# Performance work log

Measured on AMD Instinct MI355X. Metric: run time of the kernel, lower is better.

## Reference

```python
import jax, jax.numpy as jnp
import numpy as np

B, T, D = 64, 512, 1024

def setup_inputs() -> dict:
    key = jax.random.key(0)
    k1, k2, k3 = jax.random.split(key, 3)
    q1 = jax.random.normal(k1, (B, T, D), dtype=jnp.float32)
    q2 = jax.random.normal(k2, (B, T, D), dtype=jnp.float32)
    # original uses 'uniform' init; scale like a small uniform weight
    U = jax.random.uniform(k3, (D, D), dtype=jnp.float32, minval=-0.05, maxval=0.05)
    return {"q1": q1, "q2": q2, "U": U}

def reference(q1, q2, U):
    # bilinear scores: (q1 @ U) @ q2^T -> [B, T1, T2]
    att = jnp.einsum('btd,de,bse->bts', q1, U, q2)
    att = jax.nn.relu(att)
    w1_att = jax.nn.softmax(att, axis=1)  # softmax over q1 timesteps
    w2_att = jax.nn.softmax(att, axis=2)  # softmax over q2 timesteps
    # q1_align = w1_att^T @ q1 -> [B, T2, D]
    q1_align = jnp.einsum('bts,btd->bsd', w1_att, q1)
    # q2_align = w2_att @ q2 -> [B, T1, D]
    q2_align = jnp.einsum('bts,bsd->btd', w2_att, q2)
    return (q1_align, q2_align)
```

## Files before the change

kernel.cpp:

```cpp
#include <hip/hip_runtime.h>
#include <hip/hip_bf16.h>
#include <math.h>

#define B_DIM 64
#define T_DIM 512
#define D_DIM 1024
#define TT (T_DIM * T_DIM)
#define TD (T_DIM * D_DIM)

typedef _Float16 f16;
typedef f16 f16x4 __attribute__((ext_vector_type(4)));
typedef f16 f16x8 __attribute__((ext_vector_type(8)));
typedef float f32x4 __attribute__((ext_vector_type(4)));


__device__ __forceinline__ void gld_lds16(const void* g, void* l) {
    __builtin_amdgcn_global_load_lds(
        (const __attribute__((address_space(1))) void*)g,
        (__attribute__((address_space(3))) void*)l, 16, 0, 0);
}

template <int EPI>
__global__ __launch_bounds__(512, 2) void k_mfma2(
        const f16* __restrict__ A, int lda,
        const f16* __restrict__ Bt, int ldb, int K,
        void* __restrict__ Cout, int ldc,
        const float* __restrict__ scale,
        long batchA, long batchB, long batchC, long batchS,
        float2* __restrict__ rowP, float2* __restrict__ colP, long pstr,
        const f16* __restrict__ A2, const f16* __restrict__ Bt2,
        void* __restrict__ Cout2, const float* __restrict__ scale2, int zsplit) {
    __shared__ f16 LA[2][8192];
    __shared__ f16 LB[2][8192];

    const int tid = threadIdx.x;
    const int lane = tid & 63, w = tid >> 6;

    const int gX = gridDim.x, gY = gridDim.y;
    int nwg = gX * gY * gridDim.z;
    int o = blockIdx.x + gX * (blockIdx.y + gY * blockIdx.z);
    int q8 = nwg >> 3, r8 = nwg & 7, xcd = o & 7, idx = o >> 3;
    int fl = (xcd < r8 ? xcd * (q8 + 1) : r8 * (q8 + 1) + (xcd - r8) * q8) + idx;
    const int bx = fl % gX;
    int tmp = fl / gX;
    const int by = tmp % gY;
    const int bz = tmp / gY;

    const f16* Au = A; const f16* Bu = Bt;
    void* Cu = Cout; const float* su = scale;
    int zb = bz;
    if constexpr (EPI == 2) {
        if (bz >= zsplit) {
            zb = bz - zsplit;
            Au = A2; Bu = Bt2; Cu = Cout2; su = scale2;
        }
    }

    const f16* Ab = Au + (long)zb * batchA + (long)(by * 256) * lda;
    const f16* Bb = Bu + (long)zb * batchB + (long)(bx * 256) * ldb;

    const int r0 = tid >> 2, s0 = (tid & 3) ^ (r0 & 3);
    const int r1 = (512 + tid) >> 2, s1 = ((512 + tid) & 3) ^ (r1 & 3);
    const long offA0 = (long)r0 * lda + s0 * 8;
    const long offA1 = (long)r1 * lda + s1 * 8;
    const long offB0 = (long)r0 * ldb + s0 * 8;
    const long offB1 = (long)r1 * ldb + s1 * 8;
    const int ldsOff0 = w * 512;
    const int ldsOff1 = 4096 + w * 512;

    const int g = lane >> 4;
    const int rA0 = (w & 1) * 128 + (lane & 15);
    const int rB0 = (w >> 1) * 64 + (lane & 15);

    f32x4 acc[8][4] = {};

    gld_lds16(Ab + offA0, &LA[0][ldsOff0]);
    gld_lds16(Ab + offA1, &LA[0][ldsOff1]);
    gld_lds16(Bb + offB0, &LB[0][ldsOff0]);
    gld_lds16(Bb + offB1, &LB[0][ldsOff1]);
    __syncthreads();

    const int NT = K >> 5;
    for (int t = 0; t < NT; ++t) {
        const int cur = t & 1;
        if (t + 1 < NT) {
            const long kt = (long)(t + 1) << 5;
            gld_lds16(Ab + offA0 + kt, &LA[cur ^ 1][ldsOff0]);
            gld_lds16(Ab + offA1 + kt, &LA[cur ^ 1][ldsOff1]);
            gld_lds16(Bb + offB0 + kt, &LB[cur ^ 1][ldsOff0]);
            gld_lds16(Bb + offB1 + kt, &LB[cur ^ 1][ldsOff1]);
        }
        f16x8 a[8], b[4];
#pragma unroll
        for (int m = 0; m < 8; ++m) {
            int r = rA0 + m * 16;
            a[m] = *(const f16x8*)(&LA[cur][r * 32 + ((g ^ (r & 3)) << 3)]);
        }
#pragma unroll
        for (int n = 0; n < 4; ++n) {
            int r = rB0 + n * 16;
            b[n] = *(const f16x8*)(&LB[cur][r * 32 + ((g ^ (r & 3)) << 3)]);
        }
#pragma unroll
        for (int m = 0; m < 8; ++m)
#pragma unroll
            for (int n = 0; n < 4; ++n)
                acc[m][n] = __builtin_amdgcn_mfma_f32_16x16x32_f16(a[m], b[n], acc[m][n], 0, 0, 0);
        __syncthreads();
    }

    const int row0 = by * 256 + (w & 1) * 128 + (lane >> 4) * 4;
    const int col0 = bx * 256 + (w >> 1) * 64 + (lane & 15);

    if constexpr (EPI == 0) {
        f16* C = (f16*)Cu;
#pragma unroll
        for (int m = 0; m < 8; ++m)
#pragma unroll
            for (int r = 0; r < 4; ++r) {
                long row = row0 + m * 16 + r;
#pragma unroll
                for (int n = 0; n < 4; ++n)
                    C[row * ldc + col0 + n * 16] = (f16)acc[m][n][r];
            }
    } else if constexpr (EPI == 1) {
#pragma unroll
        for (int m = 0; m < 8; ++m)
#pragma unroll
            for (int n = 0; n < 4; ++n)
#pragma unroll
                for (int r = 0; r < 4; ++r)
                    acc[m][n][r] = fmaxf(acc[m][n][r], 0.0f);
        float* C = (float*)Cu + (long)zb * batchC;
#pragma unroll
        for (int m = 0; m < 8; ++m)
#pragma unroll
            for (int r = 0; r < 4; ++r) {
                long row = row0 + m * 16 + r;
#pragma unroll
                for (int n = 0; n < 4; ++n)
                    C[row * ldc + col0 + n * 16] = acc[m][n][r];
            }
        float* redR = (float*)(&LA[0][0]);
        float* redC = redR + 2048;
        const int h = w & 1, cw = w >> 1;
#pragma unroll
        for (int m = 0; m < 8; ++m)
#pragma unroll
            for (int r = 0; r < 4; ++r) {
                float mx = fmaxf(fmaxf(acc[m][0][r], acc[m][1][r]),
                                 fmaxf(acc[m][2][r], acc[m][3][r]));
                mx = fmaxf(mx, __shfl_xor(mx, 1));
                mx = fmaxf(mx, __shfl_xor(mx, 2));
                mx = fmaxf(mx, __shfl_xor(mx, 4));
                mx = fmaxf(mx, __shfl_xor(mx, 8));
                float sm = __expf(acc[m][0][r] - mx) + __expf(acc[m][1][r] - mx)
                         + __expf(acc[m][2][r] - mx) + __expf(acc[m][3][r] - mx);
                sm += __shfl_xor(sm, 1);
                sm += __shfl_xor(sm, 2);
                sm += __shfl_xor(sm, 4);
                sm += __shfl_xor(sm, 8);
                if ((lane & 15) == 0) {
                    int lr = m * 16 + (lane >> 4) * 4 + r;
                    redR[((h * 128 + lr) * 4 + cw) * 2 + 0] = mx;
                    redR[((h * 128 + lr) * 4 + cw) * 2 + 1] = sm;
                }
            }
#pragma unroll
        for (int n = 0; n < 4; ++n) {
            float mx = acc[0][n][0];
#pragma unroll
            for (int m = 0; m < 8; ++m)
#pragma unroll
                for (int r = 0; r < 4; ++r) mx = fmaxf(mx, acc[m][n][r]);
            mx = fmaxf(mx, __shfl_xor(mx, 16));
            mx = fmaxf(mx, __shfl_xor(mx, 32));
            float sm = 0.f;
#pragma unroll
            for (int m = 0; m < 8; ++m)
#pragma unroll
                for (int r = 0; r < 4; ++r) sm += __expf(acc[m][n][r] - mx);
            sm += __shfl_xor(sm, 16);
            sm += __shfl_xor(sm, 32);
            if (lane < 16) {
                int c = cw * 64 + n * 16 + lane;
                redC[(h * 256 + c) * 2 + 0] = mx;
                redC[(h * 256 + c) * 2 + 1] = sm;
            }
        }
        __syncthreads();
        if (tid < 256) {
            float M = -1e30f, S = 0.f;
#pragma unroll
            for (int i = 0; i < 4; ++i) {
                float m_ = redR[(tid * 4 + i) * 2 + 0];
                float s_ = redR[(tid * 4 + i) * 2 + 1];
                float nm = fmaxf(M, m_);
                S = S * __expf(M - nm) + s_ * __expf(m_ - nm);
                M = nm;
            }
            rowP[(long)bx * pstr + (long)bz * 512 + by * 256 + tid] = make_float2(M, S);
        } else {
            int c = tid - 256;
            float m0_ = redC[c * 2 + 0], s0_ = redC[c * 2 + 1];
            float m1_ = redC[(256 + c) * 2 + 0], s1_ = redC[(256 + c) * 2 + 1];
            float M = fmaxf(m0_, m1_);
            float S = s0_ * __expf(m0_ - M) + s1_ * __expf(m1_ - M);
            colP[(long)by * pstr + (long)bz * 512 + bx * 256 + c] = make_float2(M, S);
        }
    } else {
        float* C = (float*)Cu + (long)zb * batchC;
        const float* sz = su + (long)zb * batchS;
#pragma unroll
        for (int m = 0; m < 8; ++m)
#pragma unroll
            for (int r = 0; r < 4; ++r) {
                long row = row0 + m * 16 + r;
                float inv = 1.0f / sz[row];
#pragma unroll
                for (int n = 0; n < 4; ++n)
                    C[row * ldc + col0 + n * 16] = acc[m][n][r] * inv;
            }
    }
}

__global__ __launch_bounds__(256) void k_comb(const float2* __restrict__ rowP,
                                              const float2* __restrict__ colP, long pstr,
                                              float* __restrict__ rmax, float* __restrict__ rsum,
                                              float* __restrict__ cmax, float* __restrict__ csum,
                                              int b0, int n) {
    int i = blockIdx.x * 256 + threadIdx.x;
    if (i >= n) return;
    float2 a = rowP[i], b = rowP[pstr + i];
    float M = fmaxf(a.x, b.x);
    float S = a.y * __expf(a.x - M) + b.y * __expf(b.x - M);
    rmax[(size_t)b0 * T_DIM + i] = M;
    rsum[(size_t)b0 * T_DIM + i] = S;
    a = colP[i]; b = colP[pstr + i];
    M = fmaxf(a.x, b.x);
    S = a.y * __expf(a.x - M) + b.y * __expf(b.x - M);
    cmax[(size_t)b0 * T_DIM + i] = M;
    csum[(size_t)b0 * T_DIM + i] = S;
}

__global__ __launch_bounds__(256) void k_cast_both(const float* __restrict__ src,
                                                   f16* __restrict__ dst,
                                                   f16* __restrict__ dstT) {
    __shared__ f16 tr[64][72];
    int b = blockIdx.z;
    int d0 = blockIdx.x * 64, t0 = blockIdx.y * 64;
    const float* S = src + ((size_t)b * T_DIM + t0) * D_DIM + d0;
    f16* Dr = dst + ((size_t)b * T_DIM + t0) * D_DIM + d0;
    int tid = threadIdx.x;
    int rr = tid >> 4, cc = (tid & 15) * 4;
#pragma unroll
    for (int i = 0; i < 4; ++i) {
        int r = rr + i * 16;
        float4 v = *(const float4*)(S + (size_t)r * D_DIM + cc);
        f16x4 h = {(f16)v.x, (f16)v.y, (f16)v.z, (f16)v.w};
        *(f16x4*)(Dr + (size_t)r * D_DIM + cc) = h;
        tr[cc + 0][r] = h[0];
        tr[cc + 1][r] = h[1];
        tr[cc + 2][r] = h[2];
        tr[cc + 3][r] = h[3];
    }
    __syncthreads();
    f16* Dt = dstT + ((size_t)b * D_DIM + d0) * T_DIM + t0;
    int r2 = tid >> 3, c8 = (tid & 7) * 8;
#pragma unroll
    for (int i = 0; i < 2; ++i) {
        int d = r2 + i * 32;
        f16x8 vv = *(const f16x8*)(&tr[d][c8]);
        *(f16x8*)(Dt + (size_t)d * T_DIM + c8) = vv;
    }
}

__global__ __launch_bounds__(256) void k_castU(const float* __restrict__ U,
                                               f16* __restrict__ Uht) {
    __shared__ f16 tr[64][72];
    int n0 = blockIdx.x * 64, k0 = blockIdx.y * 64;
    int tid = threadIdx.x;
    int rr = tid >> 4, cc = (tid & 15) * 4;
#pragma unroll
    for (int i = 0; i < 4; ++i) {
        int r = rr + i * 16;
        float4 v = *(const float4*)(U + (size_t)(k0 + r) * D_DIM + n0 + cc);
        tr[cc + 0][r] = (f16)v.x;
        tr[cc + 1][r] = (f16)v.y;
        tr[cc + 2][r] = (f16)v.z;
        tr[cc + 3][r] = (f16)v.w;
    }
    __syncthreads();
    int r2 = tid >> 3, c8 = (tid & 7) * 8;
#pragma unroll
    for (int i = 0; i < 2; ++i) {
        int n = r2 + i * 32;
        f16x8 vv = *(const f16x8*)(&tr[n][c8]);
        *(f16x8*)(Uht + (size_t)(n0 + n) * D_DIM + k0 + c8) = vv;
    }
}

__global__ __launch_bounds__(256) void k_pconv(const float* __restrict__ att,
                                               const float* __restrict__ rmax,
                                               const float* __restrict__ cmax,
                                               f16* __restrict__ P2, f16* __restrict__ P1,
                                               int b0) {
    __shared__ f16 tr[64][72];
    int z = blockIdx.z;
    int t0 = blockIdx.y * 64, s0 = blockIdx.x * 64;
    const float* S = att + (size_t)z * TT + (size_t)t0 * T_DIM + s0;
    const float* rm = rmax + (size_t)(b0 + z) * T_DIM + t0;
    const float* cm = cmax + (size_t)(b0 + z) * T_DIM + s0;
    int tid = threadIdx.x;
    int rr = tid >> 4, cc = (tid & 15) * 4;
#pragma unroll
    for (int i = 0; i < 4; ++i) {
        int r = rr + i * 16;
        float4 v = *(const float4*)(S + (size_t)r * T_DIM + cc);
        float m = rm[r];
        f16x4 p2 = {(f16)__expf(v.x - m), (f16)__expf(v.y - m),
                    (f16)__expf(v.z - m), (f16)__expf(v.w - m)};
        *(f16x4*)(P2 + (size_t)z * TT + (size_t)(t0 + r) * T_DIM + s0 + cc) = p2;
        float4 c4 = *(const float4*)(cm + cc);
        tr[cc + 0][r] = (f16)__expf(v.x - c4.x);
        tr[cc + 1][r] = (f16)__expf(v.y - c4.y);
        tr[cc + 2][r] = (f16)__expf(v.z - c4.z);
        tr[cc + 3][r] = (f16)__expf(v.w - c4.w);
    }
    __syncthreads();
    int r2 = tid >> 3, c8 = (tid & 7) * 8;
#pragma unroll
    for (int i = 0; i < 2; ++i) {
        int s = r2 + i * 32;
        f16x8 vv = *(const f16x8*)(&tr[s][c8]);
        *(f16x8*)(P1 + (size_t)z * TT + (size_t)(s0 + s) * T_DIM + t0 + c8) = vv;
    }
}

__global__ __launch_bounds__(256) void k_rowstats(const float* __restrict__ att,
                                                  float* __restrict__ rmax,
                                                  float* __restrict__ rsum, int b0) {
    int wave = threadIdx.x >> 6, lane = threadIdx.x & 63;
    int lr = blockIdx.x * 4 + wave;
    const float4* row = reinterpret_cast<const float4*>(att + (size_t)lr * T_DIM);
    float4 v0 = row[lane];
    float4 v1 = row[lane + 64];
    float m = fmaxf(fmaxf(fmaxf(v0.x, v0.y), fmaxf(v0.z, v0.w)),
                    fmaxf(fmaxf(v1.x, v1.y), fmaxf(v1.z, v1.w)));
#pragma unroll
    for (int off = 32; off >= 1; off >>= 1) m = fmaxf(m, __shfl_xor(m, off));
    float s = __expf(v0.x - m) + __expf(v0.y - m) + __expf(v0.z - m) + __expf(v0.w - m)
            + __expf(v1.x - m) + __expf(v1.y - m) + __expf(v1.z - m) + __expf(v1.w - m);
#pragma unroll
    for (int off = 32; off >= 1; off >>= 1) s += __shfl_xor(s, off);
    if (lane == 0) {
        size_t gr = (size_t)b0 * T_DIM + lr;
        rmax[gr] = m;
        rsum[gr] = s;
    }
}

__global__ __launch_bounds__(256) void k_colstats(const float* __restrict__ att,
                                                  float* __restrict__ cmax,
                                                  float* __restrict__ csum, int b0) {
    int lb = blockIdx.y;
    int s = blockIdx.x * 256 + threadIdx.x;
    const float* base = att + (size_t)lb * TT + s;
    float m = -INFINITY, sum = 0.f;
    for (int t = 0; t < T_DIM; ++t) {
        float x = base[(size_t)t * T_DIM];
        float nm = fmaxf(m, x);
        sum = sum * __expf(m - nm) + __expf(x - nm);
        m = nm;
    }
    size_t g = (size_t)(b0 + lb) * T_DIM + s;
    cmax[g] = m;
    csum[g] = sum;
}

#define BM 128
#define BN 128
#define BKK 16
#define APITCH 132

__device__ __forceinline__ void stage_a_rowmajor(float* As, const float* __restrict__ A,
                                                 int lda, int tid) {
#pragma unroll
    for (int i = 0; i < 2; ++i) {
        int idx = tid + i * 256;
        int r = idx >> 2;
        int k4 = (idx & 3) << 2;
        float4 v = *reinterpret_cast<const float4*>(&A[(size_t)r * lda + k4]);
        As[(k4 + 0) * APITCH + r] = v.x;
        As[(k4 + 1) * APITCH + r] = v.y;
        As[(k4 + 2) * APITCH + r] = v.z;
        As[(k4 + 3) * APITCH + r] = v.w;
    }
}
__device__ __forceinline__ void stage_a_rowmajor_exp(float* As, const float* __restrict__ A,
                                                     int lda, const float* __restrict__ rowmax,
                                                     int tid) {
#pragma unroll
    for (int i = 0; i < 2; ++i) {
        int idx = tid + i * 256;
        int r = idx >> 2;
        int k4 = (idx & 3) << 2;
        float4 v = *reinterpret_cast<const float4*>(&A[(size_t)r * lda + k4]);
        float m = rowmax[r];
        As[(k4 + 0) * APITCH + r] = __expf(v.x - m);
        As[(k4 + 1) * APITCH + r] = __expf(v.y - m);
        As[(k4 + 2) * APITCH + r] = __expf(v.z - m);
        As[(k4 + 3) * APITCH + r] = __expf(v.w - m);
    }
}
__device__ __forceinline__ void stage_a_colmajor_exp(float* As, const float* __restrict__ S,
                                                     int lds, const float* __restrict__ colmax,
                                                     int tid) {
#pragma unroll
    for (int i = 0; i < 2; ++i) {
        int idx = tid + i * 256;
        int k = idx >> 5;
        int m4 = (idx & 31) << 2;
        float4 v = *reinterpret_cast<const float4*>(&S[(size_t)k * lds + m4]);
        float4 c = *reinterpret_cast<const float4*>(&colmax[m4]);
        float4 o;
        o.x = __expf(v.x - c.x); o.y = __expf(v.y - c.y);
        o.z = __expf(v.z - c.z); o.w = __expf(v.w - c.w);
        *reinterpret_cast<float4*>(&As[k * APITCH + m4]) = o;
    }
}
__device__ __forceinline__ void stage_b_rowmajor(float* Bs, const float* __restrict__ Bp,
                                                 int ldb, int tid) {
#pragma unroll
    for (int i = 0; i < 2; ++i) {
        int idx = tid + i * 256;
        int k = idx >> 5;
        int c4 = idx & 31;
        float4 v = *reinterpret_cast<const float4*>(&Bp[(size_t)k * ldb + (c4 << 2)]);
        *reinterpret_cast<float4*>(&Bs[k * BN + ((c4 & 1) << 6) + ((c4 >> 1) << 2)]) = v;
    }
}
__device__ __forceinline__ void stage_b_transpose(float* Bs, const float* __restrict__ Q,
                                                  int ldq, int tid) {
#pragma unroll
    for (int i = 0; i < 2; ++i) {
        int idx = tid + i * 256;
        int s = idx >> 2;
        int e4 = (idx & 3) << 2;
        float4 v = *reinterpret_cast<const float4*>(&Q[(size_t)s * ldq + e4]);
        int sw = ((s & 4) << 4) + ((s >> 3) << 2) + (s & 3);
        Bs[(e4 + 0) * BN + sw] = v.x;
        Bs[(e4 + 1) * BN + sw] = v.y;
        Bs[(e4 + 2) * BN + sw] = v.z;
        Bs[(e4 + 3) * BN + sw] = v.w;
    }
}
__device__ __forceinline__ void gemm_inner(const float* As, const float* Bs,
                                           float acc[8][8], int tx, int ty) {
#pragma unroll
    for (int k = 0; k < BKK; ++k) {
        float4 a0 = *reinterpret_cast<const float4*>(&As[k * APITCH + ty * 8]);
        float4 a1 = *reinterpret_cast<const float4*>(&As[k * APITCH + ty * 8 + 4]);
        float4 b0 = *reinterpret_cast<const float4*>(&Bs[k * BN + tx * 4]);
        float4 b1 = *reinterpret_cast<const float4*>(&Bs[k * BN + 64 + tx * 4]);
        float a[8] = {a0.x, a0.y, a0.z, a0.w, a1.x, a1.y, a1.z, a1.w};
        float b[8] = {b0.x, b0.y, b0.z, b0.w, b1.x, b1.y, b1.z, b1.w};
#pragma unroll
        for (int i = 0; i < 8; ++i)
#pragma unroll
            for (int j = 0; j < 8; ++j)
                acc[i][j] = fmaf(a[i], b[j], acc[i][j]);
    }
}
__global__ __launch_bounds__(256) void k_gemm_qU(const float* __restrict__ q1,
                                                 const float* __restrict__ U,
                                                 float* __restrict__ qU, int b0) {
    __shared__ float As[BKK * APITCH];
    __shared__ float Bs[BKK * BN];
    int tid = threadIdx.x, tx = tid & 15, ty = tid >> 4;
    int m0 = blockIdx.y * BM;
    int n0 = blockIdx.x * BN;
    const float* Abase = q1 + (size_t)b0 * TD + (size_t)m0 * D_DIM;
    const float* Bbase = U + n0;
    float acc[8][8] = {};
    for (int kt = 0; kt < D_DIM; kt += BKK) {
        stage_a_rowmajor(As, Abase + kt, D_DIM, tid);
        stage_b_rowmajor(Bs, Bbase + (size_t)kt * D_DIM, D_DIM, tid);
        __syncthreads();
        gemm_inner(As, Bs, acc, tx, ty);
        __syncthreads();
    }
    float* Cp = qU + (size_t)m0 * D_DIM + n0;
#pragma unroll
    for (int i = 0; i < 8; ++i) {
        int r = ty * 8 + i;
        float4 o0 = {acc[i][0], acc[i][1], acc[i][2], acc[i][3]};
        float4 o1 = {acc[i][4], acc[i][5], acc[i][6], acc[i][7]};
        *reinterpret_cast<float4*>(&Cp[(size_t)r * D_DIM + tx * 8]) = o0;
        *reinterpret_cast<float4*>(&Cp[(size_t)r * D_DIM + tx * 8 + 4]) = o1;
    }
}
__global__ __launch_bounds__(256) void k_att(const float* __restrict__ qU,
                                             const float* __restrict__ q2,
                                             float* __restrict__ att, int b0) {
    __shared__ float As[BKK * APITCH];
    __shared__ float Bs[BKK * BN];
    int tid = threadIdx.x, tx = tid & 15, ty = tid >> 4;
    int lb = blockIdx.z;
    int m0 = blockIdx.y * BM;
    int n0 = blockIdx.x * BN;
    const float* Abase = qU + (size_t)lb * TD + (size_t)m0 * D_DIM;
    const float* Qbase = q2 + (size_t)(b0 + lb) * TD + (size_t)n0 * D_DIM;
    float acc[8][8] = {};
    for (int kt = 0; kt < D_DIM; kt += BKK) {
        stage_a_rowmajor(As, Abase + kt, D_DIM, tid);
        stage_b_transpose(Bs, Qbase + kt, D_DIM, tid);
        __syncthreads();
        gemm_inner(As, Bs, acc, tx, ty);
        __syncthreads();
    }
    float* Cp = att + (size_t)lb * TT + (size_t)m0 * T_DIM + n0;
#pragma unroll
    for (int i = 0; i < 8; ++i) {
        int r = ty * 8 + i;
        float4 o0 = {fmaxf(acc[i][0], 0.f), fmaxf(acc[i][1], 0.f), fmaxf(acc[i][2], 0.f), fmaxf(acc[i][3], 0.f)};
        float4 o1 = {fmaxf(acc[i][4], 0.f), fmaxf(acc[i][5], 0.f), fmaxf(acc[i][6], 0.f), fmaxf(acc[i][7], 0.f)};
        *reinterpret_cast<float4*>(&Cp[(size_t)r * T_DIM + tx * 8]) = o0;
        *reinterpret_cast<float4*>(&Cp[(size_t)r * T_DIM + tx * 8 + 4]) = o1;
    }
}
__global__ __launch_bounds__(256) void k_q2align(const float* __restrict__ att,
                                                 const float* __restrict__ q2,
                                                 const float* __restrict__ rmax,
                                                 const float* __restrict__ rsum,
                                                 float* __restrict__ out, int b0) {
    __shared__ float As[BKK * APITCH];
    __shared__ float Bs[BKK * BN];
    int tid = threadIdx.x, tx = tid & 15, ty = tid >> 4;
    int lb = blockIdx.z;
    int m0 = blockIdx.y * BM;
    int n0 = blockIdx.x * BN;
    const float* Abase = att + (size_t)lb * TT + (size_t)m0 * T_DIM;
    const float* rmaxp = rmax + (size_t)(b0 + lb) * T_DIM + m0;
    const float* rsump = rsum + (size_t)(b0 + lb) * T_DIM + m0;
    const float* Bbase = q2 + (size_t)(b0 + lb) * TD + n0;
    float acc[8][8] = {};
    for (int kt = 0; kt < T_DIM; kt += BKK) {
        stage_a_rowmajor_exp(As, Abase + kt, T_DIM, rmaxp, tid);
        stage_b_rowmajor(Bs, Bbase + (size_t)kt * D_DIM, D_DIM, tid);
        __syncthreads();
        gemm_inner(As, Bs, acc, tx, ty);
        __syncthreads();
    }
    float* Cp = out + (size_t)B_DIM * TD + (size_t)(b0 + lb) * TD + (size_t)m0 * D_DIM + n0;
#pragma unroll
    for (int i = 0; i < 8; ++i) {
        int r = ty * 8 + i;
        float inv = 1.0f / rsump[r];
        float4 o0 = {acc[i][0] * inv, acc[i][1] * inv, acc[i][2] * inv, acc[i][3] * inv};
        float4 o1 = {acc[i][4] * inv, acc[i][5] * inv, acc[i][6] * inv, acc[i][7] * inv};
        *reinterpret_cast<float4*>(&Cp[(size_t)r * D_DIM + tx * 8]) = o0;
        *reinterpret_cast<float4*>(&Cp[(size_t)r * D_DIM + tx * 8 + 4]) = o1;
    }
}
__global__ __launch_bounds__(256) void k_q1align(const float* __restrict__ att,
                                                 const float* __restrict__ q1,
                                                 const float* __restrict__ cmax,
                                                 const float* __restrict__ csum,
                                                 float* __restrict__ out, int b0) {
    __shared__ float As[BKK * APITCH];
    __shared__ float Bs[BKK * BN];
    int tid = threadIdx.x, tx = tid & 15, ty = tid >> 4;
    int lb = blockIdx.z;
    int m0 = blockIdx.y * BM;
    int n0 = blockIdx.x * BN;
    const float* Sbase = att + (size_t)lb * TT + m0;
    const float* cmaxp = cmax + (size_t)(b0 + lb) * T_DIM + m0;
    const float* csump = csum + (size_t)(b0 + lb) * T_DIM + m0;
    const float* Bbase = q1 + (size_t)(b0 + lb) * TD + n0;
    float acc[8][8] = {};
    for (int kt = 0; kt < T_DIM; kt += BKK) {
        stage_a_colmajor_exp(As, Sbase + (size_t)kt * T_DIM, T_DIM, cmaxp, tid);
        stage_b_rowmajor(Bs, Bbase + (size_t)kt * D_DIM, D_DIM, tid);
        __syncthreads();
        gemm_inner(As, Bs, acc, tx, ty);
        __syncthreads();
    }
    float* Cp = out + (size_t)(b0 + lb) * TD + (size_t)m0 * D_DIM + n0;
#pragma unroll
    for (int i = 0; i < 8; ++i) {
        int r = ty * 8 + i;
        float inv = 1.0f / csump[r];
        float4 o0 = {acc[i][0] * inv, acc[i][1] * inv, acc[i][2] * inv, acc[i][3] * inv};
        float4 o1 = {acc[i][4] * inv, acc[i][5] * inv, acc[i][6] * inv, acc[i][7] * inv};
        *reinterpret_cast<float4*>(&Cp[(size_t)r * D_DIM + tx * 8]) = o0;
        *reinterpret_cast<float4*>(&Cp[(size_t)r * D_DIM + tx * 8 + 4]) = o1;
    }
}

extern "C" void kernel_launch(void* const* d_in, const int* in_sizes, int n_in,
                              void* d_out, int out_size, void* d_ws, size_t ws_size,
                              hipStream_t stream) {
    const float* q1 = (const float*)d_in[0];
    const float* q2 = (const float*)d_in[1];
    const float* U  = (const float*)d_in[2];
    float* out = (float*)d_out;

    const size_t BT  = (size_t)B_DIM * T_DIM;
    const size_t BTD = (size_t)B_DIM * TD;
    const size_t DD  = (size_t)D_DIM * D_DIM;

    const size_t fixedB = BT * 4 * 4
                        + (4 * BTD + DD) * 2;
    const size_t perbB  = (size_t)TD * 2 + (size_t)TT * 4 + (size_t)TT * 4
                        + 4ull * T_DIM * sizeof(float2);
    int C = 64;
    while (C > 1 && fixedB + (size_t)C * perbB > ws_size) C >>= 1;

    if (fixedB + perbB <= ws_size) {
        float* rmax = (float*)d_ws;
        float* rsum = rmax + BT;
        float* cmax = rsum + BT;
        float* csum = cmax + BT;
        f16* q1h  = (f16*)(csum + BT);
        f16* q1ht = q1h  + BTD;
        f16* q2h  = q1ht + BTD;
        f16* q2ht = q2h  + BTD;
        f16* Uht  = q2ht + BTD;
        f16* qUh  = Uht  + DD;
        float* att = (float*)(qUh + (size_t)C * TD);
        f16* P2h  = (f16*)(att + (size_t)C * TT);
        f16* P1h  = P2h + (size_t)C * TT;
        float2* rowP = (float2*)(P1h + (size_t)C * TT);
        float2* colP = rowP + 2ull * C * T_DIM;
        const long pstr = (long)C * T_DIM;

        k_cast_both<<<dim3(16, 8, 64), 256, 0, stream>>>(q1, q1h, q1ht);
        k_cast_both<<<dim3(16, 8, 64), 256, 0, stream>>>(q2, q2h, q2ht);
        k_castU<<<dim3(16, 16), 256, 0, stream>>>(U, Uht);

        for (int b0 = 0; b0 < B_DIM; b0 += C) {
            k_mfma2<0><<<dim3(4, C * 2, 1), 512, 0, stream>>>(
                q1h + (size_t)b0 * TD, D_DIM, Uht, D_DIM, D_DIM,
                qUh, D_DIM, nullptr, 0, 0, 0, 0,
                nullptr, nullptr, 0, nullptr, nullptr, nullptr, nullptr, 0);
            k_mfma2<1><<<dim3(2, 2, C), 512, 0, stream>>>(
                qUh, D_DIM, q2h + (size_t)b0 * TD, D_DIM, D_DIM,
                att, T_DIM, nullptr, (long)TD, (long)TD, (long)TT, 0,
                rowP, colP, pstr, nullptr, nullptr, nullptr, nullptr, 0);
            k_comb<<<dim3((C * T_DIM + 255) / 256), 256, 0, stream>>>(
                rowP, colP, pstr, rmax, rsum, cmax, csum, b0, C * T_DIM);
            k_pconv<<<dim3(8, 8, C), 256, 0, stream>>>(att, rmax, cmax, P2h, P1h, b0);
            k_mfma2<2><<<dim3(4, 2, 2 * C), 512, 0, stream>>>(
                P2h, T_DIM, q2ht + (size_t)b0 * TD, T_DIM, T_DIM,
                out + BTD + (size_t)b0 * TD, D_DIM, rsum + (size_t)b0 * T_DIM,
                (long)TT, (long)TD, (long)TD, T_DIM,
                nullptr, nullptr, 0,
                P1h, q1ht + (size_t)b0 * TD,
                out + (size_t)b0 * TD, csum + (size_t)b0 * T_DIM, C);
        }
        return;
    }

    const size_t statsElems = 4ull * B_DIM * T_DIM;
    float* rmax = (float*)d_ws;
    float* rsum = rmax + BT;
    float* cmax = rsum + BT;
    float* csum = cmax + BT;
    float* scratch = csum + BT;
    size_t availFloats = (ws_size > statsElems * 4) ? (ws_size - statsElems * 4) / 4 : 0;
    int C2 = 64;
    while (C2 > 1 && (size_t)C2 * (TD + TT) > availFloats) C2 >>= 1;
    if ((size_t)C2 * (TD + TT) > availFloats) return;
    float* qU  = scratch;
    float* att = qU + (size_t)C2 * TD;
    for (int b0 = 0; b0 < B_DIM; b0 += C2) {
        k_gemm_qU<<<dim3(D_DIM / BN, C2 * (T_DIM / BM)), 256, 0, stream>>>(q1, U, qU, b0);
        k_att<<<dim3(T_DIM / BN, T_DIM / BM, C2), 256, 0, stream>>>(qU, q2, att, b0);
        k_rowstats<<<dim3(C2 * T_DIM / 4), 256, 0, stream>>>(att, rmax, rsum, b0);
        k_colstats<<<dim3(T_DIM / 256, C2), 256, 0, stream>>>(att, cmax, csum, b0);
        k_q2align<<<dim3(D_DIM / BN, T_DIM / BM, C2), 256, 0, stream>>>(att, q2, rmax, rsum, out, b0);
        k_q1align<<<dim3(D_DIM / BN, T_DIM / BM, C2), 256, 0, stream>>>(att, q1, cmax, csum, out, b0);
    }
}
```

Measured before the change: 451.8 us.

## Fuse softmax partial combine into consumers, merge cast launches, change LDS swizzle

Removes the separate k_comb kernel. The row/column partial (max, sum) pairs are now combined inline, in k_pconv for the maxima and in the final GEMM epilogue for the sums. The two q1/q2 cast launches become one launch over a doubled z grid. The LDS XOR swizzle also changes from r&3 to (r>>1)&3, which targets bank conflicts in the f16x8 fragment reads. The trade-off is that the combine arithmetic is recomputed redundantly in every consumer block, in exchange for fewer launches and less stats traffic.

```diff
diff --git a/kernel.cpp b/kernel.cpp
--- a/kernel.cpp
+++ b/kernel.cpp
@@ -20,16 +20,18 @@
         (__attribute__((address_space(3))) void*)l, 16, 0, 0);
 }
 
+#define SWZ(r) (((r) >> 1) & 3)
+
 template <int EPI>
 __global__ __launch_bounds__(512, 2) void k_mfma2(
         const f16* __restrict__ A, int lda,
         const f16* __restrict__ Bt, int ldb, int K,
         void* __restrict__ Cout, int ldc,
-        const float* __restrict__ scale,
-        long batchA, long batchB, long batchC, long batchS,
+        const float2* __restrict__ scaleP,
+        long batchA, long batchB, long batchC,
         float2* __restrict__ rowP, float2* __restrict__ colP, long pstr,
         const f16* __restrict__ A2, const f16* __restrict__ Bt2,
-        void* __restrict__ Cout2, const float* __restrict__ scale2, int zsplit) {
+        void* __restrict__ Cout2, const float2* __restrict__ scaleP2, int zsplit) {
     __shared__ f16 LA[2][8192];
     __shared__ f16 LB[2][8192];
 
@@ -47,20 +49,20 @@
     const int bz = tmp / gY;
 
     const f16* Au = A; const f16* Bu = Bt;
-    void* Cu = Cout; const float* su = scale;
+    void* Cu = Cout; const float2* su = scaleP;
     int zb = bz;
     if constexpr (EPI == 2) {
         if (bz >= zsplit) {
             zb = bz - zsplit;
-            Au = A2; Bu = Bt2; Cu = Cout2; su = scale2;
+            Au = A2; Bu = Bt2; Cu = Cout2; su = scaleP2;
         }
     }
 
     const f16* Ab = Au + (long)zb * batchA + (long)(by * 256) * lda;
     const f16* Bb = Bu + (long)zb * batchB + (long)(bx * 256) * ldb;
 
-    const int r0 = tid >> 2, s0 = (tid & 3) ^ (r0 & 3);
-    const int r1 = (512 + tid) >> 2, s1 = ((512 + tid) & 3) ^ (r1 & 3);
+    const int r0 = tid >> 2, s0 = (tid & 3) ^ SWZ(r0);
+    const int r1 = (512 + tid) >> 2, s1 = ((512 + tid) & 3) ^ SWZ(r1);
     const long offA0 = (long)r0 * lda + s0 * 8;
     const long offA1 = (long)r1 * lda + s1 * 8;
     const long offB0 = (long)r0 * ldb + s0 * 8;
@@ -94,12 +96,12 @@
 #pragma unroll
         for (int m = 0; m < 8; ++m) {
             int r = rA0 + m * 16;
-            a[m] = *(const f16x8*)(&LA[cur][r * 32 + ((g ^ (r & 3)) << 3)]);
+            a[m] = *(const f16x8*)(&LA[cur][r * 32 + ((g ^ SWZ(r)) << 3)]);
         }
 #pragma unroll
         for (int n = 0; n < 4; ++n) {
             int r = rB0 + n * 16;
-            b[n] = *(const f16x8*)(&LB[cur][r * 32 + ((g ^ (r & 3)) << 3)]);
+            b[n] = *(const f16x8*)(&LB[cur][r * 32 + ((g ^ SWZ(r)) << 3)]);
         }
 #pragma unroll
         for (int m = 0; m < 8; ++m)
@@ -210,13 +212,16 @@
         }
     } else {
         float* C = (float*)Cu + (long)zb * batchC;
-        const float* sz = su + (long)zb * batchS;
+        const float2* sp = su + (long)zb * 512;
 #pragma unroll
         for (int m = 0; m < 8; ++m)
 #pragma unroll
             for (int r = 0; r < 4; ++r) {
                 long row = row0 + m * 16 + r;
-                float inv = 1.0f / sz[row];
+                float2 pa = sp[row], pb = sp[pstr + row];
+                float M = fmaxf(pa.x, pb.x);
+                float S = pa.y * __expf(pa.x - M) + pb.y * __expf(pb.x - M);
+                float inv = 1.0f / S;
 #pragma unroll
                 for (int n = 0; n < 4; ++n)
                     C[row * ldc + col0 + n * 16] = acc[m][n][r] * inv;
@@ -224,30 +229,16 @@
     }
 }
 
-__global__ __launch_bounds__(256) void k_comb(const float2* __restrict__ rowP,
-                                              const float2* __restrict__ colP, long pstr,
-                                              float* __restrict__ rmax, float* __restrict__ rsum,
-                                              float* __restrict__ cmax, float* __restrict__ csum,
-                                              int b0, int n) {
-    int i = blockIdx.x * 256 + threadIdx.x;
-    if (i >= n) return;
-    float2 a = rowP[i], b = rowP[pstr + i];
-    float M = fmaxf(a.x, b.x);
-    float S = a.y * __expf(a.x - M) + b.y * __expf(b.x - M);
-    rmax[(size_t)b0 * T_DIM + i] = M;
-    rsum[(size_t)b0 * T_DIM + i] = S;
-    a = colP[i]; b = colP[pstr + i];
-    M = fmaxf(a.x, b.x);
-    S = a.y * __expf(a.x - M) + b.y * __expf(b.x - M);
-    cmax[(size_t)b0 * T_DIM + i] = M;
-    csum[(size_t)b0 * T_DIM + i] = S;
-}
-
-__global__ __launch_bounds__(256) void k_cast_both(const float* __restrict__ src,
-                                                   f16* __restrict__ dst,
-                                                   f16* __restrict__ dstT) {
+__global__ __launch_bounds__(256) void k_cast_both(const float* __restrict__ q1,
+                                                   const float* __restrict__ q2,
+                                                   f16* __restrict__ q1h, f16* __restrict__ q1ht,
+                                                   f16* __restrict__ q2h, f16* __restrict__ q2ht) {
     __shared__ f16 tr[64][72];
-    int b = blockIdx.z;
+    int zz = blockIdx.z;
+    int b = zz & 63;
+    const float* src = (zz < 64) ? q1 : q2;
+    f16* dst  = (zz < 64) ? q1h : q2h;
+    f16* dstT = (zz < 64) ? q1ht : q2ht;
     int d0 = blockIdx.x * 64, t0 = blockIdx.y * 64;
     const float* S = src + ((size_t)b * T_DIM + t0) * D_DIM + d0;
     f16* Dr = dst + ((size_t)b * T_DIM + t0) * D_DIM + d0;
@@ -301,31 +292,39 @@
 }
 
 __global__ __launch_bounds__(256) void k_pconv(const float* __restrict__ att,
-                                               const float* __restrict__ rmax,
-                                               const float* __restrict__ cmax,
-                                               f16* __restrict__ P2, f16* __restrict__ P1,
-                                               int b0) {
+                                               const float2* __restrict__ rowP,
+                                               const float2* __restrict__ colP, long pstr,
+                                               f16* __restrict__ P2, f16* __restrict__ P1) {
     __shared__ f16 tr[64][72];
+    __shared__ float rmS[64], cmS[64];
     int z = blockIdx.z;
     int t0 = blockIdx.y * 64, s0 = blockIdx.x * 64;
+    int tid = threadIdx.x;
+    if (tid < 64) {
+        float2 a = rowP[(long)z * 512 + t0 + tid];
+        float2 b = rowP[pstr + (long)z * 512 + t0 + tid];
+        rmS[tid] = fmaxf(a.x, b.x);
+    } else if (tid < 128) {
+        int s = tid - 64;
+        float2 a = colP[(long)z * 512 + s0 + s];
+        float2 b = colP[pstr + (long)z * 512 + s0 + s];
+        cmS[s] = fmaxf(a.x, b.x);
+    }
+    __syncthreads();
     const float* S = att + (size_t)z * TT + (size_t)t0 * T_DIM + s0;
-    const float* rm = rmax + (size_t)(b0 + z) * T_DIM + t0;
-    const float* cm = cmax + (size_t)(b0 + z) * T_DIM + s0;
-    int tid = threadIdx.x;
     int rr = tid >> 4, cc = (tid & 15) * 4;
 #pragma unroll
     for (int i = 0; i < 4; ++i) {
         int r = rr + i * 16;
         float4 v = *(const float4*)(S + (size_t)r * T_DIM + cc);
-        float m = rm[r];
+        float m = rmS[r];
         f16x4 p2 = {(f16)__expf(v.x - m), (f16)__expf(v.y - m),
                     (f16)__expf(v.z - m), (f16)__expf(v.w - m)};
         *(f16x4*)(P2 + (size_t)z * TT + (size_t)(t0 + r) * T_DIM + s0 + cc) = p2;
-        float4 c4 = *(const float4*)(cm + cc);
-        tr[cc + 0][r] = (f16)__expf(v.x - c4.x);
-        tr[cc + 1][r] = (f16)__expf(v.y - c4.y);
-        tr[cc + 2][r] = (f16)__expf(v.z - c4.z);
-        tr[cc + 3][r] = (f16)__expf(v.w - c4.w);
+        tr[cc + 0][r] = (f16)__expf(v.x - cmS[cc + 0]);
+        tr[cc + 1][r] = (f16)__expf(v.y - cmS[cc + 1]);
+        tr[cc + 2][r] = (f16)__expf(v.z - cmS[cc + 2]);
+        tr[cc + 3][r] = (f16)__expf(v.w - cmS[cc + 3]);
     }
     __syncthreads();
     int r2 = tid >> 3, c8 = (tid & 7) * 8;
@@ -610,19 +609,14 @@
     const size_t BTD = (size_t)B_DIM * TD;
     const size_t DD  = (size_t)D_DIM * D_DIM;
 
-    const size_t fixedB = BT * 4 * 4
-                        + (4 * BTD + DD) * 2;
+    const size_t fixedB = (4 * BTD + DD) * 2;
     const size_t perbB  = (size_t)TD * 2 + (size_t)TT * 4 + (size_t)TT * 4
                         + 4ull * T_DIM * sizeof(float2);
     int C = 64;
     while (C > 1 && fixedB + (size_t)C * perbB > ws_size) C >>= 1;
 
     if (fixedB + perbB <= ws_size) {
-        float* rmax = (float*)d_ws;
-        float* rsum = rmax + BT;
-        float* cmax = rsum + BT;
-        float* csum = cmax + BT;
-        f16* q1h  = (f16*)(csum + BT);
+        f16* q1h  = (f16*)d_ws;
         f16* q1ht = q1h  + BTD;
         f16* q2h  = q1ht + BTD;
         f16* q2ht = q2h  + BTD;
@@ -635,29 +629,26 @@
         float2* colP = rowP + 2ull * C * T_DIM;
         const long pstr = (long)C * T_DIM;
 
-        k_cast_both<<<dim3(16, 8, 64), 256, 0, stream>>>(q1, q1h, q1ht);
-        k_cast_both<<<dim3(16, 8, 64), 256, 0, stream>>>(q2, q2h, q2ht);
+        k_cast_both<<<dim3(16, 8, 128), 256, 0, stream>>>(q1, q2, q1h, q1ht, q2h, q2ht);
         k_castU<<<dim3(16, 16), 256, 0, stream>>>(U, Uht);
 
         for (int b0 = 0; b0 < B_DIM; b0 += C) {
             k_mfma2<0><<<dim3(4, C * 2, 1), 512, 0, stream>>>(
                 q1h + (size_t)b0 * TD, D_DIM, Uht, D_DIM, D_DIM,
-                qUh, D_DIM, nullptr, 0, 0, 0, 0,
+                qUh, D_DIM, nullptr, 0, 0, 0,
                 nullptr, nullptr, 0, nullptr, nullptr, nullptr, nullptr, 0);
             k_mfma2<1><<<dim3(2, 2, C), 512, 0, stream>>>(
                 qUh, D_DIM, q2h + (size_t)b0 * TD, D_DIM, D_DIM,
-                att, T_DIM, nullptr, (long)TD, (long)TD, (long)TT, 0,
+                att, T_DIM, nullptr, (long)TD, (long)TD, (long)TT,
                 rowP, colP, pstr, nullptr, nullptr, nullptr, nullptr, 0);
-            k_comb<<<dim3((C * T_DIM + 255) / 256), 256, 0, stream>>>(
-                rowP, colP, pstr, rmax, rsum, cmax, csum, b0, C * T_DIM);
-            k_pconv<<<dim3(8, 8, C), 256, 0, stream>>>(att, rmax, cmax, P2h, P1h, b0);
+            k_pconv<<<dim3(8, 8, C), 256, 0, stream>>>(att, rowP, colP, pstr, P2h, P1h);
             k_mfma2<2><<<dim3(4, 2, 2 * C), 512, 0, stream>>>(
                 P2h, T_DIM, q2ht + (size_t)b0 * TD, T_DIM, T_DIM,
-                out + BTD + (size_t)b0 * TD, D_DIM, rsum + (size_t)b0 * T_DIM,
-                (long)TT, (long)TD, (long)TD, T_DIM,
-                nullptr, nullptr, 0,
+                out + BTD + (size_t)b0 * TD, D_DIM, rowP,
+                (long)TT, (long)TD, (long)TD,
+                nullptr, nullptr, pstr,
                 P1h, q1ht + (size_t)b0 * TD,
-                out + (size_t)b0 * TD, csum + (size_t)b0 * T_DIM, C);
+                out + (size_t)b0 * TD, colP, C);
         }
         return;
     }
```

Result: no change. 452.5 us (+0.2%).
